# Kernel tuning notes

Hardware: AMD Instinct MI355X
Metric: run time of the kernel (lower is better)

## Reference

```python
import jax, jax.numpy as jnp
import numpy as np

NEG_INF_SCALE = -1e9


def multihead(q_in, kv_in, W, b, mask):
    # W: [3, H, d, dh] (q, k, v); b: [3, H, dh]
    q = jnp.einsum('bsd,hdk->bhsk', q_in, W[0]) + b[0][None, :, None, :]
    k = jnp.einsum('bsd,hdk->bhsk', kv_in, W[1]) + b[1][None, :, None, :]
    v = jnp.einsum('bsd,hdk->bhsk', kv_in, W[2]) + b[2][None, :, None, :]
    dh = q.shape[-1]
    scores = jnp.einsum('bhqd,bhkd->bhqk', q, k) / jnp.sqrt(jnp.float32(dh))
    if mask is not None:
        scores = scores + mask * NEG_INF_SCALE  # mask==1 at disallowed positions
    attn = jax.nn.softmax(scores, axis=-1)
    out = jnp.einsum('bhqk,bhkd->bhqd', attn, v)
    B, H, S, DH = out.shape
    # concat of per-head outputs along last axis == transpose + reshape
    return out.transpose(0, 2, 1, 3).reshape(B, S, H * DH)


def setup_inputs() -> dict:
    key = jax.random.key(0)
    ks = jax.random.split(key, 8)
    B, S, D, H, DH, DFF = 8, 1024, 1024, 16, 64, 2048
    sc_in = 1.0 / np.sqrt(D)
    sc_ff = 1.0 / np.sqrt(DFF)
    de_x = jax.random.normal(ks[0], (B, S, D), jnp.float32)
    en_x = jax.random.normal(ks[1], (B, S, D), jnp.float32)
    # causal mask: 1 at masked (future) positions
    mask = jnp.triu(jnp.ones((S, S), jnp.float32), k=1)
    attn1_w = jax.random.normal(ks[2], (3, H, D, DH), jnp.float32) * sc_in
    attn1_b = jnp.zeros((3, H, DH), jnp.float32)
    attn2_w = jax.random.normal(ks[3], (3, H, D, DH), jnp.float32) * sc_in
    attn2_b = jnp.zeros((3, H, DH), jnp.float32)
    ffn_w1 = jax.random.normal(ks[4], (D, DFF), jnp.float32) * sc_in
    ffn_b1 = jnp.zeros((DFF,), jnp.float32)
    ffn_w2 = jax.random.normal(ks[5], (DFF, D), jnp.float32) * sc_ff
    ffn_b2 = jnp.zeros((D,), jnp.float32)
    return {'de_x': de_x, 'en_x': en_x, 'mask': mask,
            'attn1_w': attn1_w, 'attn1_b': attn1_b,
            'attn2_w': attn2_w, 'attn2_b': attn2_b,
            'ffn_w1': ffn_w1, 'ffn_b1': ffn_b1,
            'ffn_w2': ffn_w2, 'ffn_b2': ffn_b2}


def reference(de_x, en_x, mask, attn1_w, attn1_b, attn2_w, attn2_b,
              ffn_w1, ffn_b1, ffn_w2, ffn_b2):
    # block 1: K=V=en_x, Q=de_x, masked (as in source: head(en_x, en_x, de_x, mask))
    h1 = multihead(de_x, en_x, attn1_w, attn1_b, mask)
    # block 2: K=V=en_x, Q=h1, no mask
    h2 = multihead(h1, en_x, attn2_w, attn2_b, None)
    # FCLayer(2048, d): d -> 2048 relu -> d
    y = jax.nn.relu(h2 @ ffn_w1 + ffn_b1) @ ffn_w2 + ffn_b2
    return y
```

## Files before the change

kernel.cpp:

```cpp
#include <hip/hip_runtime.h>

typedef unsigned short u16;
typedef __attribute__((ext_vector_type(8))) __bf16 bf16x8;
typedef __attribute__((ext_vector_type(4))) float f32x4;

__device__ __forceinline__ u16 f2bf(float f) {
    unsigned int u = __builtin_bit_cast(unsigned int, f);
    u = (u + 0x7fffu + ((u >> 16) & 1u)) >> 16;
    return (u16)u;
}

typedef __attribute__((address_space(1))) const void gv_t;
typedef __attribute__((address_space(3))) void lv_t;
__device__ __forceinline__ void gl_lds16(const void* g, void* l) {
    __builtin_amdgcn_global_load_lds((gv_t*)g, (lv_t*)l, 16, 0, 0);
}

__global__ __launch_bounds__(256) void cvt_bf16_k(const float* __restrict__ in,
                                                  u16* __restrict__ out, int n4) {
    int i = blockIdx.x * 256 + threadIdx.x;
    if (i >= n4) return;
    float4 f = ((const float4*)in)[i];
    ushort4 o;
    o.x = f2bf(f.x); o.y = f2bf(f.y); o.z = f2bf(f.z); o.w = f2bf(f.w);
    ((ushort4*)out)[i] = o;
}

__global__ __launch_bounds__(256) void pack_attn_w_k(const float* __restrict__ W,
                                                     u16* __restrict__ out) {
    int idx = blockIdx.x * 256 + threadIdx.x;
    int kk = idx & 63;
    int d  = (idx >> 6) & 1023;
    int h  = (idx >> 16) & 15;
    int p  = idx >> 20;
    out[p * 1048576 + (h * 64 + kk) * 1024 + d] = f2bf(W[idx]);
}

__global__ __launch_bounds__(256) void transpose_bf16_k(const float* __restrict__ in,
                                                        u16* __restrict__ out, int R, int C) {
    int idx = blockIdx.x * 256 + threadIdx.x;
    if (idx >= R * C) return;
    int r = idx / C, c = idx - r * C;
    out[c * R + r] = f2bf(in[idx]);
}

template <int RELU, int OUTF32>
__global__ __launch_bounds__(256) void gemm_bt_k(const u16* __restrict__ A,
                                                 const u16* __restrict__ Bt,
                                                 const float* __restrict__ bias,
                                                 u16* __restrict__ Obf,
                                                 float* __restrict__ Of,
                                                 int M, int N, int K, float scale) {
    __shared__ u16 As[128 * 32];
    __shared__ u16 Bs[128 * 32];
    const int tid = threadIdx.x, lane = tid & 63, w = tid >> 6;
    const int wr = w >> 1, wc = w & 1;
    const int m0 = blockIdx.y * 128, n0 = blockIdx.x * 128;
    const int rowA = lane >> 2;
    const int colk = (lane & 3) * 8;

    f32x4 acc[4][4] = {};

    for (int k0 = 0; k0 < K; k0 += 32) {
        for (int q = 0; q < 2; ++q) {
            int seg = w * 2 + q;
            gl_lds16(A  + (size_t)(m0 + seg * 16 + rowA) * K + k0 + colk, &As[seg * 512]);
            gl_lds16(Bt + (size_t)(n0 + seg * 16 + rowA) * K + k0 + colk, &Bs[seg * 512]);
        }
        __syncthreads();
        bf16x8 a[4], b[4];
        #pragma unroll
        for (int m = 0; m < 4; ++m)
            a[m] = *(const bf16x8*)&As[(wr * 64 + m * 16 + (lane & 15)) * 32 + (lane >> 4) * 8];
        #pragma unroll
        for (int n = 0; n < 4; ++n)
            b[n] = *(const bf16x8*)&Bs[(wc * 64 + n * 16 + (lane & 15)) * 32 + (lane >> 4) * 8];
        #pragma unroll
        for (int m = 0; m < 4; ++m)
            #pragma unroll
            for (int n = 0; n < 4; ++n)
                acc[m][n] = __builtin_amdgcn_mfma_f32_16x16x32_bf16(a[m], b[n], acc[m][n], 0, 0, 0);
        __syncthreads();
    }

    #pragma unroll
    for (int m = 0; m < 4; ++m)
        #pragma unroll
        for (int n = 0; n < 4; ++n) {
            int col = n0 + wc * 64 + n * 16 + (lane & 15);
            float bv = bias[col];
            #pragma unroll
            for (int i = 0; i < 4; ++i) {
                int row = m0 + wr * 64 + m * 16 + (lane >> 4) * 4 + i;
                float v = acc[m][n][i] + bv;
                if (RELU) v = fmaxf(v, 0.f);
                v *= scale;
                if (OUTF32) Of[(size_t)row * N + col] = v;
                else        Obf[(size_t)row * N + col] = f2bf(v);
            }
        }
}

__global__ __launch_bounds__(256) void gemm_proj_k(const u16* __restrict__ Ade,
                                                   const u16* __restrict__ Aen,
                                                   const u16* __restrict__ W,
                                                   const float* __restrict__ b1,
                                                   const float* __restrict__ b2,
                                                   u16* __restrict__ Qb,
                                                   u16* __restrict__ Kb1, u16* __restrict__ Vt1,
                                                   u16* __restrict__ Kb2, u16* __restrict__ Vt2) {
    const int K = 1024;
    __shared__ u16 As[128 * 32];
    __shared__ u16 Bs[128 * 32];
    const int tid = threadIdx.x, lane = tid & 63, w = tid >> 6;
    const int wr = w >> 1, wc = w & 1;
    const int xt = blockIdx.x;
    const int n0 = (xt < 24 ? xt : xt + 8) * 128;
    const int seg = n0 >> 10;
    const int m0 = blockIdx.y * 128;
    const u16* A  = (seg == 0) ? Ade : Aen;
    const u16* Bt = W + (size_t)n0 * K;
    const float* bias = (seg < 3) ? (b1 + seg * 1024) : (b2 + (seg - 3) * 1024);
    const int nb = n0 & 1023;
    const int rowA = lane >> 2;
    const int colk = (lane & 3) * 8;

    f32x4 acc[4][4] = {};

    for (int k0 = 0; k0 < K; k0 += 32) {
        for (int q = 0; q < 2; ++q) {
            int sg = w * 2 + q;
            gl_lds16(A  + (size_t)(m0 + sg * 16 + rowA) * K + k0 + colk, &As[sg * 512]);
            gl_lds16(Bt + (size_t)(sg * 16 + rowA) * K + k0 + colk, &Bs[sg * 512]);
        }
        __syncthreads();
        bf16x8 a[4], b[4];
        #pragma unroll
        for (int m = 0; m < 4; ++m)
            a[m] = *(const bf16x8*)&As[(wr * 64 + m * 16 + (lane & 15)) * 32 + (lane >> 4) * 8];
        #pragma unroll
        for (int n = 0; n < 4; ++n)
            b[n] = *(const bf16x8*)&Bs[(wc * 64 + n * 16 + (lane & 15)) * 32 + (lane >> 4) * 8];
        #pragma unroll
        for (int m = 0; m < 4; ++m)
            #pragma unroll
            for (int n = 0; n < 4; ++n)
                acc[m][n] = __builtin_amdgcn_mfma_f32_16x16x32_bf16(a[m], b[n], acc[m][n], 0, 0, 0);
        __syncthreads();
    }

    const int isV = (seg == 2 || seg == 5);
    u16* Orow = (seg == 0) ? Qb : (seg == 1 ? Kb1 : Kb2);
    u16* Ovt  = (seg == 2) ? Vt1 : Vt2;
    const float scale = (seg == 0) ? 0.125f : 1.0f;

    #pragma unroll
    for (int m = 0; m < 4; ++m)
        #pragma unroll
        for (int n = 0; n < 4; ++n) {
            int col = nb + wc * 64 + n * 16 + (lane & 15);
            float bv = bias[col];
            int row0 = m0 + wr * 64 + m * 16 + (lane >> 4) * 4;
            if (isV) {
                ushort4 o;
                o.x = f2bf(acc[m][n][0] + bv);
                o.y = f2bf(acc[m][n][1] + bv);
                o.z = f2bf(acc[m][n][2] + bv);
                o.w = f2bf(acc[m][n][3] + bv);
                size_t off = ((size_t)((row0 >> 10) * 16 + (col >> 6)) * 64 + (col & 63)) * 1024
                             + (row0 & 1023);
                *(ushort4*)&Ovt[off] = o;
            } else {
                #pragma unroll
                for (int i = 0; i < 4; ++i) {
                    float v = (acc[m][n][i] + bv) * scale;
                    Orow[(size_t)(row0 + i) * 1024 + col] = f2bf(v);
                }
            }
        }
}

template <int CAUSAL>
__global__ __launch_bounds__(256) void attn_k(const u16* __restrict__ Q,
                                              const u16* __restrict__ Kg_,
                                              const u16* __restrict__ Vt_,
                                              u16* __restrict__ O, int S) {
    const int HD = 1024;
    __shared__ u16 Kl[2][4096];
    __shared__ u16 Vl[2][4096];
    __shared__ u16 Pl[4][16 * 72];
    const int tid = threadIdx.x, lane = tid & 63, w = tid >> 6;
    const int qt = blockIdx.x, h = blockIdx.y, b = blockIdx.z;
    const u16* Qg  = Q   + ((size_t)b * S) * HD + h * 64;
    const u16* Kgp = Kg_ + ((size_t)b * S) * HD + h * 64;
    const u16* Vtp = Vt_ + (size_t)(b * 16 + h) * 64 * 1024;
    const int q0 = qt * 64 + w * 16;
    const int l15 = lane & 15, l4 = lane >> 4;
    const int sr = lane >> 3, sc = lane & 7;

    bf16x8 aq[2];
    #pragma unroll
    for (int kc = 0; kc < 2; ++kc)
        aq[kc] = *(const bf16x8*)&Qg[(size_t)(q0 + l15) * HD + kc * 32 + l4 * 8];

    f32x4 acc_o[4] = {};
    float mrow[4], lrow[4];
    #pragma unroll
    for (int i = 0; i < 4; ++i) { mrow[i] = -3.0e38f; lrow[i] = 0.f; }
    u16* Pw = Pl[w];

    const int nkb = CAUSAL ? (qt + 1) : (S / 64);

    {
        const int k0 = 0;
        #pragma unroll
        for (int qq = 0; qq < 2; ++qq) {
            int rbase = w * 16 + qq * 8;
            int r = rbase + sr;
            int cs = sc ^ (r & 7);
            gl_lds16(Kgp + (size_t)(k0 + r) * HD + cs * 8, (void*)&Kl[0][rbase * 64]);
            gl_lds16(Vtp + (size_t)r * 1024 + k0 + cs * 8, (void*)&Vl[0][rbase * 64]);
        }
    }
    __syncthreads();

    int buf = 0;
    for (int kb = 0; kb < nkb; ++kb) {
        if (kb + 1 < nkb) {
            const int k0n = (kb + 1) * 64;
            #pragma unroll
            for (int qq = 0; qq < 2; ++qq) {
                int rbase = w * 16 + qq * 8;
                int r = rbase + sr;
                int cs = sc ^ (r & 7);
                gl_lds16(Kgp + (size_t)(k0n + r) * HD + cs * 8, (void*)&Kl[buf ^ 1][rbase * 64]);
                gl_lds16(Vtp + (size_t)r * 1024 + k0n + cs * 8, (void*)&Vl[buf ^ 1][rbase * 64]);
            }
        }
        const u16* Kc = Kl[buf];
        const u16* Vc = Vl[buf];

        f32x4 accs[4] = {};
        #pragma unroll
        for (int ct = 0; ct < 4; ++ct) {
            int row = ct * 16 + l15;
            #pragma unroll
            for (int kc = 0; kc < 2; ++kc) {
                int g = kc * 4 + l4;
                bf16x8 bk = *(const bf16x8*)&Kc[row * 64 + (g ^ (row & 7)) * 8];
                accs[ct] = __builtin_amdgcn_mfma_f32_16x16x32_bf16(aq[kc], bk, accs[ct], 0, 0, 0);
            }
        }

        float vals[4][4], tmax[4];
        #pragma unroll
        for (int i = 0; i < 4; ++i) tmax[i] = -3.0e38f;
        if (CAUSAL && kb == qt) {
            #pragma unroll
            for (int ct = 0; ct < 4; ++ct)
                #pragma unroll
                for (int i = 0; i < 4; ++i) {
                    float v = accs[ct][i];
                    int kr = ct * 16 + l15;
                    int qr = w * 16 + l4 * 4 + i;
                    if (kr > qr) v = -1.0e9f;
                    vals[ct][i] = v;
                    tmax[i] = fmaxf(tmax[i], v);
                }
        } else {
            #pragma unroll
            for (int ct = 0; ct < 4; ++ct)
                #pragma unroll
                for (int i = 0; i < 4; ++i) {
                    float v = accs[ct][i];
                    vals[ct][i] = v;
                    tmax[i] = fmaxf(tmax[i], v);
                }
        }
        #pragma unroll
        for (int off = 1; off < 16; off <<= 1)
            #pragma unroll
            for (int i = 0; i < 4; ++i) tmax[i] = fmaxf(tmax[i], __shfl_xor(tmax[i], off));

        float scale[4], rsum[4];
        #pragma unroll
        for (int i = 0; i < 4; ++i) {
            float mn = fmaxf(mrow[i], tmax[i]);
            scale[i] = __expf(mrow[i] - mn);
            mrow[i] = mn;
            rsum[i] = 0.f;
        }
        #pragma unroll
        for (int ct = 0; ct < 4; ++ct)
            #pragma unroll
            for (int i = 0; i < 4; ++i) {
                float p = __expf(vals[ct][i] - mrow[i]);
                vals[ct][i] = p;
                rsum[i] += p;
            }
        #pragma unroll
        for (int off = 1; off < 16; off <<= 1)
            #pragma unroll
            for (int i = 0; i < 4; ++i) rsum[i] += __shfl_xor(rsum[i], off);
        #pragma unroll
        for (int i = 0; i < 4; ++i) lrow[i] = lrow[i] * scale[i] + rsum[i];
        #pragma unroll
        for (int dt = 0; dt < 4; ++dt)
            #pragma unroll
            for (int i = 0; i < 4; ++i) acc_o[dt][i] *= scale[i];

        #pragma unroll
        for (int ct = 0; ct < 4; ++ct)
            #pragma unroll
            for (int i = 0; i < 4; ++i)
                Pw[(l4 * 4 + i) * 72 + ct * 16 + l15] = f2bf(vals[ct][i]);

        #pragma unroll
        for (int kc2 = 0; kc2 < 2; ++kc2) {
            bf16x8 pa = *(const bf16x8*)&Pw[l15 * 72 + kc2 * 32 + l4 * 8];
            #pragma unroll
            for (int dt = 0; dt < 4; ++dt) {
                int row = dt * 16 + l15;
                int g = kc2 * 4 + l4;
                bf16x8 bv = *(const bf16x8*)&Vc[row * 64 + (g ^ (row & 7)) * 8];
                acc_o[dt] = __builtin_amdgcn_mfma_f32_16x16x32_bf16(pa, bv, acc_o[dt], 0, 0, 0);
            }
        }
        __syncthreads();
        buf ^= 1;
    }

    #pragma unroll
    for (int dt = 0; dt < 4; ++dt)
        #pragma unroll
        for (int i = 0; i < 4; ++i) {
            float o = acc_o[dt][i] / lrow[i];
            O[(size_t)(b * S + q0 + l4 * 4 + i) * HD + h * 64 + dt * 16 + l15] = f2bf(o);
        }
}

extern "C" void kernel_launch(void* const* d_in, const int* in_sizes, int n_in,
                              void* d_out, int out_size, void* d_ws, size_t ws_size,
                              hipStream_t stream) {
    const float* de_x = (const float*)d_in[0];
    const float* en_x = (const float*)d_in[1];
    const float* a1w  = (const float*)d_in[3];
    const float* a1b  = (const float*)d_in[4];
    const float* a2w  = (const float*)d_in[5];
    const float* a2b  = (const float*)d_in[6];
    const float* fw1  = (const float*)d_in[7];
    const float* fb1  = (const float*)d_in[8];
    const float* fw2  = (const float*)d_in[9];
    const float* fb2  = (const float*)d_in[10];
    float* out = (float*)d_out;
    u16* ws = (u16*)d_ws;

    u16* bf_de = ws + 0;
    u16* bf_en = ws + 8388608;
    u16* wproj = ws + 16777216;
    u16* wf1t  = ws + 23068672;
    u16* wf2t  = ws + 25165824;
    u16* Qb    = ws + 27262976;
    u16* Kb1   = ws + 35651584;
    u16* Vt1   = ws + 44040192;
    u16* Kb2   = ws + 52428800;
    u16* Vt2   = ws + 60817408;
    u16* h1  = bf_en;
    u16* h2  = bf_de;
    u16* mid = Kb1;
    if (ws_size < (size_t)69206016 * 2) return;

    const int M = 8192;
    dim3 blk(256);

    cvt_bf16_k<<<8192, blk, 0, stream>>>(de_x, bf_de, 2097152);
    cvt_bf16_k<<<8192, blk, 0, stream>>>(en_x, bf_en, 2097152);
    pack_attn_w_k<<<12288, blk, 0, stream>>>(a1w, wproj);
    pack_attn_w_k<<<12288, blk, 0, stream>>>(a2w, wproj + 3145728);
    transpose_bf16_k<<<8192, blk, 0, stream>>>(fw1, wf1t, 1024, 2048);
    transpose_bf16_k<<<8192, blk, 0, stream>>>(fw2, wf2t, 2048, 1024);

    gemm_proj_k<<<dim3(40, 64), blk, 0, stream>>>(bf_de, bf_en, wproj, a1b, a2b,
                                                  Qb, Kb1, Vt1, Kb2, Vt2);
    attn_k<1><<<dim3(16, 16, 8), blk, 0, stream>>>(Qb, Kb1, Vt1, h1, 1024);

    gemm_bt_k<0, 0><<<dim3(8, 64), blk, 0, stream>>>(h1, wproj + 3145728, a2b,
                                                     Qb, nullptr, M, 1024, 1024, 0.125f);
    attn_k<0><<<dim3(16, 16, 8), blk, 0, stream>>>(Qb, Kb2, Vt2, h2, 1024);

    gemm_bt_k<1, 0><<<dim3(16, 64), blk, 0, stream>>>(h2, wf1t, fb1, mid, nullptr,
                                                      M, 2048, 1024, 1.0f);
    gemm_bt_k<0, 1><<<dim3(8, 64), blk, 0, stream>>>(mid, wf2t, fb2, nullptr, out,
                                                     M, 1024, 2048, 1.0f);
}
```

Measured before the change: 711.9 us.

## Replace 128x128 GEMMs with 256x256 double-buffered swizzled LDS pipelined GEMM core

Replaces the simple 128x128, K=32-step GEMM kernels, which synchronise on every step, with a shared 256x256-tile core. It uses 512 threads, 64-wide K slabs in double-buffered XOR-swizzled LDS, and staged global_load_lds prefetches interleaved with MFMA quarters using explicit waitcnt/barriers and s_setprio. The goal is better data reuse, fewer LDS bank conflicts, and overlap of memory loads with compute for all projection and FFN GEMMs. The larger tiles leave fewer blocks (e.g. 128 for the 1024-wide GEMMs), which risks under-filling the GPU, and the hand-written vmcnt accounting is fragile.

```diff
diff --git a/kernel.cpp b/kernel.cpp
--- a/kernel.cpp
+++ b/kernel.cpp
@@ -44,138 +44,188 @@
     out[c * R + r] = f2bf(in[idx]);
 }
 
-template <int RELU, int OUTF32>
-__global__ __launch_bounds__(256) void gemm_bt_k(const u16* __restrict__ A,
-                                                 const u16* __restrict__ Bt,
-                                                 const float* __restrict__ bias,
-                                                 u16* __restrict__ Obf,
-                                                 float* __restrict__ Of,
-                                                 int M, int N, int K, float scale) {
-    __shared__ u16 As[128 * 32];
-    __shared__ u16 Bs[128 * 32];
-    const int tid = threadIdx.x, lane = tid & 63, w = tid >> 6;
-    const int wr = w >> 1, wc = w & 1;
-    const int m0 = blockIdx.y * 128, n0 = blockIdx.x * 128;
-    const int rowA = lane >> 2;
-    const int colk = (lane & 3) * 8;
-
-    f32x4 acc[4][4] = {};
-
-    for (int k0 = 0; k0 < K; k0 += 32) {
-        for (int q = 0; q < 2; ++q) {
-            int seg = w * 2 + q;
-            gl_lds16(A  + (size_t)(m0 + seg * 16 + rowA) * K + k0 + colk, &As[seg * 512]);
-            gl_lds16(Bt + (size_t)(n0 + seg * 16 + rowA) * K + k0 + colk, &Bs[seg * 512]);
-        }
-        __syncthreads();
-        bf16x8 a[4], b[4];
-        #pragma unroll
-        for (int m = 0; m < 4; ++m)
-            a[m] = *(const bf16x8*)&As[(wr * 64 + m * 16 + (lane & 15)) * 32 + (lane >> 4) * 8];
-        #pragma unroll
-        for (int n = 0; n < 4; ++n)
-            b[n] = *(const bf16x8*)&Bs[(wc * 64 + n * 16 + (lane & 15)) * 32 + (lane >> 4) * 8];
-        #pragma unroll
-        for (int m = 0; m < 4; ++m)
-            #pragma unroll
-            for (int n = 0; n < 4; ++n)
-                acc[m][n] = __builtin_amdgcn_mfma_f32_16x16x32_bf16(a[m], b[n], acc[m][n], 0, 0, 0);
-        __syncthreads();
-    }
-
+__device__ __forceinline__ void g256_core(const u16* __restrict__ Ab,
+                                          const u16* __restrict__ Bb,
+                                          int K, u16* __restrict__ As,
+                                          u16* __restrict__ Bs,
+                                          f32x4 (&acc)[8][4]) {
+    const int tid = threadIdx.x, lane = tid & 63, wid = tid >> 6;
+    const int wm = wid >> 2, wn = wid & 3;
+    const int l15 = lane & 15, l4 = lane >> 4;
+    const int gsw = (lane & 7) ^ ((lane >> 3) & 7);
+    const int lr = lane >> 3;
+
+    bf16x8 a[4][2], b[2][2];
+
+#define STG(MATb, MATs, buf, half, kt) { \
+    _Pragma("unroll") \
+    for (int j = 0; j < 2; ++j) { \
+        const int r = (half) * 128 + j * 64 + wid * 8; \
+        gl_lds16(MATb + (size_t)(r + lr) * K + (kt) * 64 + gsw * 8, \
+                 &MATs[(buf) * 16384 + r * 64]); \
+    } }
+#define LDA(buf, MLO) { \
+    _Pragma("unroll") \
+    for (int mf = 0; mf < 4; ++mf) \
+    _Pragma("unroll") \
+    for (int ks = 0; ks < 2; ++ks) \
+        a[mf][ks] = *(const bf16x8*)&As[(buf) * 16384 \
+            + (wm * 128 + ((MLO) + mf) * 16 + l15) * 64 \
+            + (((ks * 4 + l4) ^ (l15 & 7)) * 8)]; \
+    }
+#define LDB(buf, NLO) { \
+    _Pragma("unroll") \
+    for (int nf = 0; nf < 2; ++nf) \
+    _Pragma("unroll") \
+    for (int ks = 0; ks < 2; ++ks) \
+        b[nf][ks] = *(const bf16x8*)&Bs[(buf) * 16384 \
+            + (wn * 64 + ((NLO) + nf) * 16 + l15) * 64 \
+            + (((ks * 4 + l4) ^ (l15 & 7)) * 8)]; \
+    }
+#define MMA(MLO, NLO) { \
+    __builtin_amdgcn_s_setprio(1); \
+    _Pragma("unroll") \
+    for (int mf = 0; mf < 4; ++mf) \
+    _Pragma("unroll") \
+    for (int nf = 0; nf < 2; ++nf) \
+    _Pragma("unroll") \
+    for (int ks = 0; ks < 2; ++ks) \
+        acc[(MLO) + mf][(NLO) + nf] = __builtin_amdgcn_mfma_f32_16x16x32_bf16( \
+            a[mf][ks], b[nf][ks], acc[(MLO) + mf][(NLO) + nf], 0, 0, 0); \
+    __builtin_amdgcn_s_setprio(0); \
+    }
+#define BARR __builtin_amdgcn_s_barrier()
+#define LGKM0 { asm volatile("s_waitcnt lgkmcnt(0)" ::: "memory"); \
+                __builtin_amdgcn_sched_barrier(0); }
+#define WTV2 asm volatile("s_waitcnt vmcnt(2)" ::: "memory")
+#define WTV0 asm volatile("s_waitcnt vmcnt(0)" ::: "memory")
+
+    const int NI = K >> 7;
+    STG(Ab, As, 0, 0, 0); STG(Ab, As, 0, 1, 0);
+    STG(Bb, Bs, 0, 0, 0); STG(Bb, Bs, 0, 1, 0);
+    STG(Ab, As, 1, 0, 1);
+    WTV2;
+    BARR;
+
+    for (int it = 0; it < NI; ++it) {
+        const int t1 = 2 * it + 1, t2 = 2 * it + 2, t3 = 2 * it + 3;
+        const bool nl = (it + 1 < NI);
+        LDA(0, 0); LDB(0, 0);
+        STG(Ab, As, 1, 1, t1);
+        BARR; LGKM0; MMA(0, 0); BARR;
+        LDB(0, 2);
+        STG(Bb, Bs, 1, 0, t1);
+        BARR; LGKM0; MMA(0, 2); BARR;
+        LDA(0, 4); LDB(0, 0);
+        STG(Bb, Bs, 1, 1, t1);
+        BARR; LGKM0; MMA(4, 0); BARR;
+        LDB(0, 2);
+        if (nl) STG(Ab, As, 0, 0, t2);
+        BARR; LGKM0; MMA(4, 2);
+        if (nl) { WTV2; } else { WTV0; }
+        BARR;
+        LDA(1, 0); LDB(1, 0);
+        if (nl) STG(Ab, As, 0, 1, t2);
+        BARR; LGKM0; MMA(0, 0); BARR;
+        LDB(1, 2);
+        if (nl) STG(Bb, Bs, 0, 0, t2);
+        BARR; LGKM0; MMA(0, 2); BARR;
+        LDA(1, 4); LDB(1, 0);
+        if (nl) STG(Bb, Bs, 0, 1, t2);
+        BARR; LGKM0; MMA(4, 0); BARR;
+        LDB(1, 2);
+        if (nl) STG(Ab, As, 1, 0, t3);
+        BARR; LGKM0; MMA(4, 2);
+        if (nl) WTV2;
+        BARR;
+    }
+#undef STG
+#undef LDA
+#undef LDB
+#undef MMA
+#undef BARR
+#undef LGKM0
+#undef WTV2
+#undef WTV0
+}
+
+template <int MODE>
+__global__ __launch_bounds__(512, 2) void gemm256_k(const u16* __restrict__ A,
+        const u16* __restrict__ Bt, const float* __restrict__ bias,
+        u16* __restrict__ Obf, float* __restrict__ Of,
+        int M, int N, int K, float scale) {
+    __shared__ u16 As[32768];
+    __shared__ u16 Bs[32768];
+    const int m0 = blockIdx.y * 256, n0 = blockIdx.x * 256;
+    f32x4 acc[8][4] = {};
+    g256_core(A + (size_t)m0 * K, Bt + (size_t)n0 * K, K, As, Bs, acc);
+
+    const int lane = threadIdx.x & 63, wid = threadIdx.x >> 6;
+    const int wm = wid >> 2, wn = wid & 3, l15 = lane & 15, l4 = lane >> 4;
     #pragma unroll
-    for (int m = 0; m < 4; ++m)
-        #pragma unroll
-        for (int n = 0; n < 4; ++n) {
-            int col = n0 + wc * 64 + n * 16 + (lane & 15);
+    for (int mf = 0; mf < 8; ++mf)
+        #pragma unroll
+        for (int nf = 0; nf < 4; ++nf) {
+            int col = n0 + wn * 64 + nf * 16 + l15;
             float bv = bias[col];
+            int row0 = m0 + wm * 128 + mf * 16 + l4 * 4;
             #pragma unroll
             for (int i = 0; i < 4; ++i) {
-                int row = m0 + wr * 64 + m * 16 + (lane >> 4) * 4 + i;
-                float v = acc[m][n][i] + bv;
-                if (RELU) v = fmaxf(v, 0.f);
+                float v = acc[mf][nf][i] + bv;
+                if (MODE == 1) v = fmaxf(v, 0.f);
                 v *= scale;
-                if (OUTF32) Of[(size_t)row * N + col] = v;
-                else        Obf[(size_t)row * N + col] = f2bf(v);
-            }
-        }
-}
-
-__global__ __launch_bounds__(256) void gemm_proj_k(const u16* __restrict__ Ade,
-                                                   const u16* __restrict__ Aen,
-                                                   const u16* __restrict__ W,
-                                                   const float* __restrict__ b1,
-                                                   const float* __restrict__ b2,
-                                                   u16* __restrict__ Qb,
-                                                   u16* __restrict__ Kb1, u16* __restrict__ Vt1,
-                                                   u16* __restrict__ Kb2, u16* __restrict__ Vt2) {
+                if (MODE == 2) Of[(size_t)(row0 + i) * N + col] = v;
+                else           Obf[(size_t)(row0 + i) * N + col] = f2bf(v);
+            }
+        }
+}
+
+__global__ __launch_bounds__(512, 2) void gemm256_proj_k(const u16* __restrict__ Ade,
+        const u16* __restrict__ Aen, const u16* __restrict__ W,
+        const float* __restrict__ b1, const float* __restrict__ b2,
+        u16* __restrict__ Qb, u16* __restrict__ Kb1, u16* __restrict__ Vt1,
+        u16* __restrict__ Kb2, u16* __restrict__ Vt2) {
     const int K = 1024;
-    __shared__ u16 As[128 * 32];
-    __shared__ u16 Bs[128 * 32];
-    const int tid = threadIdx.x, lane = tid & 63, w = tid >> 6;
-    const int wr = w >> 1, wc = w & 1;
+    __shared__ u16 As[32768];
+    __shared__ u16 Bs[32768];
     const int xt = blockIdx.x;
-    const int n0 = (xt < 24 ? xt : xt + 8) * 128;
+    const int n0 = (xt < 12 ? xt : xt + 4) * 256;
     const int seg = n0 >> 10;
-    const int m0 = blockIdx.y * 128;
-    const u16* A  = (seg == 0) ? Ade : Aen;
-    const u16* Bt = W + (size_t)n0 * K;
+    const int m0 = blockIdx.y * 256;
+    const u16* A = (seg == 0) ? Ade : Aen;
+    f32x4 acc[8][4] = {};
+    g256_core(A + (size_t)m0 * K, W + (size_t)n0 * K, K, As, Bs, acc);
+
+    const int lane = threadIdx.x & 63, wid = threadIdx.x >> 6;
+    const int wm = wid >> 2, wn = wid & 3, l15 = lane & 15, l4 = lane >> 4;
     const float* bias = (seg < 3) ? (b1 + seg * 1024) : (b2 + (seg - 3) * 1024);
-    const int nb = n0 & 1023;
-    const int rowA = lane >> 2;
-    const int colk = (lane & 3) * 8;
-
-    f32x4 acc[4][4] = {};
-
-    for (int k0 = 0; k0 < K; k0 += 32) {
-        for (int q = 0; q < 2; ++q) {
-            int sg = w * 2 + q;
-            gl_lds16(A  + (size_t)(m0 + sg * 16 + rowA) * K + k0 + colk, &As[sg * 512]);
-            gl_lds16(Bt + (size_t)(sg * 16 + rowA) * K + k0 + colk, &Bs[sg * 512]);
-        }
-        __syncthreads();
-        bf16x8 a[4], b[4];
-        #pragma unroll
-        for (int m = 0; m < 4; ++m)
-            a[m] = *(const bf16x8*)&As[(wr * 64 + m * 16 + (lane & 15)) * 32 + (lane >> 4) * 8];
-        #pragma unroll
-        for (int n = 0; n < 4; ++n)
-            b[n] = *(const bf16x8*)&Bs[(wc * 64 + n * 16 + (lane & 15)) * 32 + (lane >> 4) * 8];
-        #pragma unroll
-        for (int m = 0; m < 4; ++m)
-            #pragma unroll
-            for (int n = 0; n < 4; ++n)
-                acc[m][n] = __builtin_amdgcn_mfma_f32_16x16x32_bf16(a[m], b[n], acc[m][n], 0, 0, 0);
-        __syncthreads();
-    }
-
     const int isV = (seg == 2 || seg == 5);
     u16* Orow = (seg == 0) ? Qb : (seg == 1 ? Kb1 : Kb2);
     u16* Ovt  = (seg == 2) ? Vt1 : Vt2;
     const float scale = (seg == 0) ? 0.125f : 1.0f;
 
     #pragma unroll
-    for (int m = 0; m < 4; ++m)
-        #pragma unroll
-        for (int n = 0; n < 4; ++n) {
-            int col = nb + wc * 64 + n * 16 + (lane & 15);
+    for (int mf = 0; mf < 8; ++mf)
+        #pragma unroll
+        for (int nf = 0; nf < 4; ++nf) {
+            int colg = n0 + wn * 64 + nf * 16 + l15;
+            int col = colg & 1023;
             float bv = bias[col];
-            int row0 = m0 + wr * 64 + m * 16 + (lane >> 4) * 4;
+            int row0 = m0 + wm * 128 + mf * 16 + l4 * 4;
             if (isV) {
                 ushort4 o;
-                o.x = f2bf(acc[m][n][0] + bv);
-                o.y = f2bf(acc[m][n][1] + bv);
-                o.z = f2bf(acc[m][n][2] + bv);
-                o.w = f2bf(acc[m][n][3] + bv);
-                size_t off = ((size_t)((row0 >> 10) * 16 + (col >> 6)) * 64 + (col & 63)) * 1024
-                             + (row0 & 1023);
+                o.x = f2bf(acc[mf][nf][0] + bv);
+                o.y = f2bf(acc[mf][nf][1] + bv);
+                o.z = f2bf(acc[mf][nf][2] + bv);
+                o.w = f2bf(acc[mf][nf][3] + bv);
+                size_t off = ((size_t)((row0 >> 10) * 16 + (col >> 6)) * 64
+                              + (col & 63)) * 1024 + (row0 & 1023);
                 *(ushort4*)&Ovt[off] = o;
             } else {
                 #pragma unroll
-                for (int i = 0; i < 4; ++i) {
-                    float v = (acc[m][n][i] + bv) * scale;
-                    Orow[(size_t)(row0 + i) * 1024 + col] = f2bf(v);
-                }
+                for (int i = 0; i < 4; ++i)
+                    Orow[(size_t)(row0 + i) * 1024 + col] =
+                        f2bf((acc[mf][nf][i] + bv) * scale);
             }
         }
 }
@@ -212,14 +262,13 @@
     const int nkb = CAUSAL ? (qt + 1) : (S / 64);
 
     {
-        const int k0 = 0;
         #pragma unroll
         for (int qq = 0; qq < 2; ++qq) {
             int rbase = w * 16 + qq * 8;
             int r = rbase + sr;
             int cs = sc ^ (r & 7);
-            gl_lds16(Kgp + (size_t)(k0 + r) * HD + cs * 8, (void*)&Kl[0][rbase * 64]);
-            gl_lds16(Vtp + (size_t)r * 1024 + k0 + cs * 8, (void*)&Vl[0][rbase * 64]);
+            gl_lds16(Kgp + (size_t)r * HD + cs * 8, (void*)&Kl[0][rbase * 64]);
+            gl_lds16(Vtp + (size_t)r * 1024 + cs * 8, (void*)&Vl[0][rbase * 64]);
         }
     }
     __syncthreads();
@@ -370,7 +419,6 @@
     u16* mid = Kb1;
     if (ws_size < (size_t)69206016 * 2) return;
 
-    const int M = 8192;
     dim3 blk(256);
 
     cvt_bf16_k<<<8192, blk, 0, stream>>>(de_x, bf_de, 2097152);
@@ -380,16 +428,16 @@
     transpose_bf16_k<<<8192, blk, 0, stream>>>(fw1, wf1t, 1024, 2048);
     transpose_bf16_k<<<8192, blk, 0, stream>>>(fw2, wf2t, 2048, 1024);
 
-    gemm_proj_k<<<dim3(40, 64), blk, 0, stream>>>(bf_de, bf_en, wproj, a1b, a2b,
-                                                  Qb, Kb1, Vt1, Kb2, Vt2);
+    gemm256_proj_k<<<dim3(20, 32), 512, 0, stream>>>(bf_de, bf_en, wproj, a1b, a2b,
+                                                     Qb, Kb1, Vt1, Kb2, Vt2);
     attn_k<1><<<dim3(16, 16, 8), blk, 0, stream>>>(Qb, Kb1, Vt1, h1, 1024);
 
-    gemm_bt_k<0, 0><<<dim3(8, 64), blk, 0, stream>>>(h1, wproj + 3145728, a2b,
-                                                     Qb, nullptr, M, 1024, 1024, 0.125f);
+    gemm256_k<0><<<dim3(4, 32), 512, 0, stream>>>(h1, wproj + 3145728, a2b,
+                                                  Qb, nullptr, 8192, 1024, 1024, 0.125f);
     attn_k<0><<<dim3(16, 16, 8), blk, 0, stream>>>(Qb, Kb2, Vt2, h2, 1024);
 
-    gemm_bt_k<1, 0><<<dim3(16, 64), blk, 0, stream>>>(h2, wf1t, fb1, mid, nullptr,
-                                                      M, 2048, 1024, 1.0f);
-    gemm_bt_k<0, 1><<<dim3(8, 64), blk, 0, stream>>>(mid, wf2t, fb2, nullptr, out,
-                                                     M, 1024, 2048, 1.0f);
-}
+    gemm256_k<1><<<dim3(8, 32), 512, 0, stream>>>(h2, wf1t, fb1, mid, nullptr,
+                                                  8192, 2048, 1024, 1.0f);
+    gemm256_k<2><<<dim3(4, 32), 512, 0, stream>>>(mid, wf2t, fb2, nullptr, out,
+                                                  8192, 1024, 2048, 1.0f);
+}
```

After: 700.3 us. No clear change (-1.6%).
